# Optimization experiments

Hardware: AMD Instinct MI355X
Metric: run time of the kernel (lower is better)

Reference implementation:

```python
import jax, jax.numpy as jnp
import numpy as np

N = 512          # data_info['n']
K = 513          # data_info['k'] + 1
B = 65536        # batch size


def _build_adjust(n, k):
    # Reproduces the __init__ mask construction exactly.
    a1 = np.ones((n - 1, k - 1, 2), dtype=np.float32)
    a2 = np.zeros((n - 1, k - 1, 2), dtype=np.float32)
    for i in range(0, k - 2):
        if i >= n - 1:
            break
        f1 = a1[i].reshape(-1)
        f1[2 + 2 * i:] = 0
        a1[i] = f1.reshape(k - 1, 2)
        f2 = a2[i].reshape(-1)
        f2[2 + 2 * i + 1] = 1
        a2[i] = f2.reshape(k - 1, 2)
    return jnp.asarray(a1), jnp.asarray(a2)


W_ADJ1, W_ADJ2 = _build_adjust(N, K)


def setup_inputs() -> dict:
    key = jax.random.key(0)
    k1, k2, k3 = jax.random.split(key, 3)
    x = jax.random.randint(k1, (B, N), 0, 2, dtype=jnp.int32)
    W = jax.random.normal(k2, (N - 1, K - 1, 2), dtype=jnp.float32)
    endW = jax.random.normal(k3, (1, K), dtype=jnp.float32)
    return {"x": x, "W": W, "endW": endW}


def reference(x, W, endW):
    # W_full construction (softmax over the 2-way split, masked, with the
    # deterministic [1,0] row prepended along the group axis).
    Wsm = jax.nn.softmax(W, axis=2)                      # (n-1, k-1, 2)
    W_full = Wsm * W_ADJ1 + W_ADJ2                       # (n-1, k-1, 2)
    append = jnp.zeros((N - 1, 1, 2), W_full.dtype).at[:, :, 0].set(1.0)
    W_full = jnp.concatenate([append, W_full], axis=1)   # (n-1, k, 2)

    # group_num at step i is the running cumsum of x[:, 0..i]; the serial
    # recurrence collapses to a single cumsum, letting us gather all steps
    # at once instead of the original n-1 step Python loop.
    g = jnp.cumsum(x, axis=1)                            # (B, n)
    steps = jnp.arange(N - 1)                            # step i -> W_full[i-1]
    vals = W_full[steps[None, :], g[:, 1:], x[:, 1:]]    # (B, n-1)
    out = jnp.sum(jnp.log(vals), axis=1, keepdims=True)  # (B, 1)

    e = jax.nn.softmax(endW, axis=1)[0]                  # (k,)
    out = out + jnp.log(e[g[:, -1]])[:, None]            # (B, 1)
    return out
```

## Files before the change

kernel.cpp:

```cpp
#include <hip/hip_runtime.h>
#include <math.h>

#define NN      512
#define KK      513
#define BB      65536
#define TROWS   512
#define TCOLS   513
#define TSTRIDE (2 * TCOLS)

#define RPB     64
#define NSEG    8
#define SEGW    64
#define BLK     (RPB * NSEG)
#define XSTR    129

typedef int iv4 __attribute__((ext_vector_type(4)));

__global__ void build_table_kernel(const float* __restrict__ W, float* __restrict__ T) {
    int idx = blockIdx.x * blockDim.x + threadIdx.x;
    if (idx >= TROWS * TCOLS) return;
    int t = idx / TCOLS;
    int g = idx - t * TCOLS;
    float v0 = 0.f, v1 = 0.f;
    if (t >= 1 && g >= 1 && g <= t) {
        const float* w = W + ((size_t)(t - 1) * (KK - 1) + (g - 1)) * 2;
        float w0 = w[0], w1 = w[1];
        float m  = fmaxf(w0, w1);
        float lse = m + logf(expf(w0 - m) + expf(w1 - m));
        v0 = w0 - lse;
        v1 = w1 - lse;
    }
    T[2 * idx + 0] = v0;
    T[2 * idx + 1] = v1;
}

__global__ void build_endw_kernel(const float* __restrict__ endW, float* __restrict__ logE) {
    int lane = threadIdx.x;
    float vals[9];
    float m = -1e30f;
    #pragma unroll
    for (int k = 0; k < 9; ++k) {
        int i = lane + 64 * k;
        vals[k] = (i < KK) ? endW[i] : -1e30f;
        m = fmaxf(m, vals[k]);
    }
    #pragma unroll
    for (int d = 32; d >= 1; d >>= 1) m = fmaxf(m, __shfl_xor(m, d, 64));
    float s = 0.f;
    #pragma unroll
    for (int k = 0; k < 9; ++k) s += expf(vals[k] - m);
    #pragma unroll
    for (int d = 32; d >= 1; d >>= 1) s += __shfl_xor(s, d, 64);
    float lse = m + logf(s);
    #pragma unroll
    for (int k = 0; k < 9; ++k) {
        int i = lane + 64 * k;
        if (i < KK) logE[i] = endW[i] - lse;
    }
}

__global__ __launch_bounds__(BLK, 8) void pc_main_kernel(
    const int* __restrict__ x, const float* __restrict__ T,
    const float* __restrict__ logE, float* __restrict__ out)
{
    __shared__ unsigned int  xb[RPB * XSTR];
    __shared__ int           segsum[NSEG * RPB];
    __shared__ float         partial[NSEG * RPB];

    const int tid  = threadIdx.x;
    const int row0 = blockIdx.x * RPB;

    {
        const iv4* tile = (const iv4*)(x + (size_t)row0 * NN);
        #pragma unroll
        for (int j = 0; j < 16; ++j) {
            int i = tid + BLK * j;
            iv4 a = __builtin_nontemporal_load(&tile[i]);
            int r    = i >> 7;
            int col4 = i & 127;
            unsigned int m = (unsigned int)(a.x & 1)
                           | ((unsigned int)(a.y & 1) << 8)
                           | ((unsigned int)(a.z & 1) << 16)
                           | ((unsigned int)(a.w & 1) << 24);
            xb[r * XSTR + col4] = m;
        }
    }
    __syncthreads();

    const int seg  = tid >> 6;
    const int lane = tid & 63;

    unsigned int w[16];
    int ssum = 0;
    #pragma unroll
    for (int m = 0; m < 16; ++m) {
        w[m] = xb[lane * XSTR + seg * 16 + m];
        ssum += __popc(w[m]);
    }
    segsum[seg * 64 + lane] = ssum;
    __syncthreads();

    int g = 0, gtot = 0;
    #pragma unroll
    for (int s = 0; s < NSEG; ++s) {
        int v = segsum[s * 64 + lane];
        if (s < seg) g += v;
        gtot += v;
    }

    float a0 = 0.f, a1 = 0.f, a2 = 0.f, a3 = 0.f;
    const float* Tbase = T + (size_t)seg * SEGW * TSTRIDE;
    #pragma unroll
    for (int m = 0; m < 16; ++m) {
        const float* Tm = Tbase + (size_t)(4 * m) * TSTRIDE;
        unsigned int wm = w[m];
        {
            int b0 = wm & 1;         g += b0; a0 += Tm[0 * TSTRIDE + 2 * g + b0];
            int b1 = (wm >> 8)  & 1; g += b1; a1 += Tm[1 * TSTRIDE + 2 * g + b1];
            int b2 = (wm >> 16) & 1; g += b2; a2 += Tm[2 * TSTRIDE + 2 * g + b2];
            int b3 = (wm >> 24) & 1; g += b3; a3 += Tm[3 * TSTRIDE + 2 * g + b3];
        }
    }
    partial[seg * 64 + lane] = (a0 + a1) + (a2 + a3);
    __syncthreads();

    if (seg == 0) {
        float s = logE[gtot];
        #pragma unroll
        for (int t = 0; t < NSEG; ++t) s += partial[t * 64 + lane];
        out[row0 + lane] = s;
    }
}

extern "C" void kernel_launch(void* const* d_in, const int* in_sizes, int n_in,
                              void* d_out, int out_size, void* d_ws, size_t ws_size,
                              hipStream_t stream)
{
    const int*   x    = (const int*)d_in[0];
    const float* W    = (const float*)d_in[1];
    const float* endW = (const float*)d_in[2];
    float*       out  = (float*)d_out;

    float* T    = (float*)d_ws;
    float* logE = (float*)((char*)d_ws + (size_t)TROWS * TCOLS * 2 * sizeof(float));

    {
        int total  = TROWS * TCOLS;
        int blocks = (total + 255) / 256;
        build_table_kernel<<<blocks, 256, 0, stream>>>(W, T);
    }
    build_endw_kernel<<<1, 64, 0, stream>>>(endW, logE);
    pc_main_kernel<<<BB / RPB, BLK, 0, stream>>>(x, T, logE, out);
}
```

Baseline: 202.0 us.

## Pack log-prob table into bf16 pairs and double-buffer two row tiles per block

New measurement: 220.8 us. +9.3%, slower.

```diff
diff --git a/kernel.cpp b/kernel.cpp
--- a/kernel.cpp
+++ b/kernel.cpp
@@ -6,17 +6,23 @@
 #define BB      65536
 #define TROWS   512
 #define TCOLS   513
-#define TSTRIDE (2 * TCOLS)
+#define T16STR  528
 
 #define RPB     64
 #define NSEG    8
 #define SEGW    64
 #define BLK     (RPB * NSEG)
 #define XSTR    129
+#define TPB2    2
 
 typedef int iv4 __attribute__((ext_vector_type(4)));
 
-__global__ void build_table_kernel(const float* __restrict__ W, float* __restrict__ T) {
+__device__ __forceinline__ unsigned f2bf(float f) {
+    unsigned u = __float_as_uint(f);
+    return (u + 0x7fffu + ((u >> 16) & 1u)) >> 16;
+}
+
+__global__ void build_table_kernel(const float* __restrict__ W, unsigned* __restrict__ T16) {
     int idx = blockIdx.x * blockDim.x + threadIdx.x;
     if (idx >= TROWS * TCOLS) return;
     int t = idx / TCOLS;
@@ -30,8 +36,7 @@
         v0 = w0 - lse;
         v1 = w1 - lse;
     }
-    T[2 * idx + 0] = v0;
-    T[2 * idx + 1] = v1;
+    T16[t * T16STR + g] = f2bf(v0) | (f2bf(v1) << 16);
 }
 
 __global__ void build_endw_kernel(const float* __restrict__ endW, float* __restrict__ logE) {
@@ -59,76 +64,97 @@
     }
 }
 
-__global__ __launch_bounds__(BLK, 8) void pc_main_kernel(
-    const int* __restrict__ x, const float* __restrict__ T,
+__global__ __launch_bounds__(BLK, 4) void pc_main_kernel(
+    const int* __restrict__ x, const unsigned* __restrict__ T16,
     const float* __restrict__ logE, float* __restrict__ out)
 {
-    __shared__ unsigned int  xb[RPB * XSTR];
-    __shared__ int           segsum[NSEG * RPB];
-    __shared__ float         partial[NSEG * RPB];
+    __shared__ unsigned xb[2][RPB * XSTR];
+    __shared__ int      segsum[NSEG * RPB];
+    __shared__ float    partial[NSEG * RPB];
 
-    const int tid  = threadIdx.x;
-    const int row0 = blockIdx.x * RPB;
+    const int tid   = threadIdx.x;
+    const int seg   = tid >> 6;
+    const int lane  = tid & 63;
+    const int rowbb = blockIdx.x * (RPB * TPB2);
 
     {
-        const iv4* tile = (const iv4*)(x + (size_t)row0 * NN);
+        const iv4* tile = (const iv4*)(x + (size_t)rowbb * NN);
         #pragma unroll
         for (int j = 0; j < 16; ++j) {
             int i = tid + BLK * j;
             iv4 a = __builtin_nontemporal_load(&tile[i]);
-            int r    = i >> 7;
-            int col4 = i & 127;
-            unsigned int m = (unsigned int)(a.x & 1)
-                           | ((unsigned int)(a.y & 1) << 8)
-                           | ((unsigned int)(a.z & 1) << 16)
-                           | ((unsigned int)(a.w & 1) << 24);
-            xb[r * XSTR + col4] = m;
+            unsigned m = (unsigned)(a.x & 1) | ((unsigned)(a.y & 1) << 8)
+                       | ((unsigned)(a.z & 1) << 16) | ((unsigned)(a.w & 1) << 24);
+            xb[0][(i >> 7) * XSTR + (i & 127)] = m;
         }
     }
     __syncthreads();
 
-    const int seg  = tid >> 6;
-    const int lane = tid & 63;
+    int cur = 0;
+    iv4 S[16];
+    #pragma unroll
+    for (int t = 0; t < TPB2; ++t) {
+        const int row0 = rowbb + t * RPB;
 
-    unsigned int w[16];
-    int ssum = 0;
-    #pragma unroll
-    for (int m = 0; m < 16; ++m) {
-        w[m] = xb[lane * XSTR + seg * 16 + m];
-        ssum += __popc(w[m]);
-    }
-    segsum[seg * 64 + lane] = ssum;
-    __syncthreads();
+        if (t + 1 < TPB2) {
+            const iv4* tile = (const iv4*)(x + (size_t)(row0 + RPB) * NN);
+            #pragma unroll
+            for (int j = 0; j < 16; ++j) S[j] = __builtin_nontemporal_load(&tile[tid + BLK * j]);
+        }
 
-    int g = 0, gtot = 0;
-    #pragma unroll
-    for (int s = 0; s < NSEG; ++s) {
-        int v = segsum[s * 64 + lane];
-        if (s < seg) g += v;
-        gtot += v;
-    }
+        unsigned w[16];
+        int ssum = 0;
+        #pragma unroll
+        for (int m = 0; m < 16; ++m) {
+            w[m] = xb[cur][lane * XSTR + seg * 16 + m];
+            ssum += __popc(w[m]);
+        }
+        segsum[seg * 64 + lane] = ssum;
+        __syncthreads();
 
-    float a0 = 0.f, a1 = 0.f, a2 = 0.f, a3 = 0.f;
-    const float* Tbase = T + (size_t)seg * SEGW * TSTRIDE;
-    #pragma unroll
-    for (int m = 0; m < 16; ++m) {
-        const float* Tm = Tbase + (size_t)(4 * m) * TSTRIDE;
-        unsigned int wm = w[m];
-        {
-            int b0 = wm & 1;         g += b0; a0 += Tm[0 * TSTRIDE + 2 * g + b0];
-            int b1 = (wm >> 8)  & 1; g += b1; a1 += Tm[1 * TSTRIDE + 2 * g + b1];
-            int b2 = (wm >> 16) & 1; g += b2; a2 += Tm[2 * TSTRIDE + 2 * g + b2];
-            int b3 = (wm >> 24) & 1; g += b3; a3 += Tm[3 * TSTRIDE + 2 * g + b3];
+        int g = 0, gtot = 0;
+        #pragma unroll
+        for (int s = 0; s < NSEG; ++s) {
+            int v = segsum[s * 64 + lane];
+            if (s < seg) g += v;
+            gtot += v;
         }
-    }
-    partial[seg * 64 + lane] = (a0 + a1) + (a2 + a3);
-    __syncthreads();
 
-    if (seg == 0) {
-        float s = logE[gtot];
+        float a0 = 0.f, a1 = 0.f, a2 = 0.f, a3 = 0.f;
+        const unsigned* Tseg = T16 + (size_t)(seg * SEGW) * T16STR;
         #pragma unroll
-        for (int t = 0; t < NSEG; ++t) s += partial[t * 64 + lane];
-        out[row0 + lane] = s;
+        for (int m = 0; m < 16; ++m) {
+            const unsigned* Tm = Tseg + (size_t)(4 * m) * T16STR;
+            unsigned wm = w[m];
+            int b0 = wm & 1;         g += b0; unsigned u0 = Tm[0 * T16STR + g];
+            a0 += __uint_as_float(b0 ? (u0 & 0xffff0000u) : (u0 << 16));
+            int b1 = (wm >> 8)  & 1; g += b1; unsigned u1 = Tm[1 * T16STR + g];
+            a1 += __uint_as_float(b1 ? (u1 & 0xffff0000u) : (u1 << 16));
+            int b2 = (wm >> 16) & 1; g += b2; unsigned u2 = Tm[2 * T16STR + g];
+            a2 += __uint_as_float(b2 ? (u2 & 0xffff0000u) : (u2 << 16));
+            int b3 = (wm >> 24) & 1; g += b3; unsigned u3 = Tm[3 * T16STR + g];
+            a3 += __uint_as_float(b3 ? (u3 & 0xffff0000u) : (u3 << 16));
+        }
+        partial[seg * 64 + lane] = (a0 + a1) + (a2 + a3);
+
+        if (t + 1 < TPB2) {
+            #pragma unroll
+            for (int j = 0; j < 16; ++j) {
+                int i = tid + BLK * j;
+                unsigned m = (unsigned)(S[j].x & 1) | ((unsigned)(S[j].y & 1) << 8)
+                           | ((unsigned)(S[j].z & 1) << 16) | ((unsigned)(S[j].w & 1) << 24);
+                xb[cur ^ 1][(i >> 7) * XSTR + (i & 127)] = m;
+            }
+        }
+        __syncthreads();
+
+        if (seg == 0) {
+            float s = logE[gtot];
+            #pragma unroll
+            for (int q = 0; q < NSEG; ++q) s += partial[q * 64 + lane];
+            out[row0 + lane] = s;
+        }
+        cur ^= 1;
     }
 }
 
@@ -141,14 +167,14 @@
     const float* endW = (const float*)d_in[2];
     float*       out  = (float*)d_out;
 
-    float* T    = (float*)d_ws;
-    float* logE = (float*)((char*)d_ws + (size_t)TROWS * TCOLS * 2 * sizeof(float));
+    unsigned* T16  = (unsigned*)d_ws;
+    float*    logE = (float*)((char*)d_ws + (size_t)TROWS * T16STR * sizeof(unsigned));
 
     {
         int total  = TROWS * TCOLS;
         int blocks = (total + 255) / 256;
-        build_table_kernel<<<blocks, 256, 0, stream>>>(W, T);
+        build_table_kernel<<<blocks, 256, 0, stream>>>(W, T16);
     }
     build_endw_kernel<<<1, 64, 0, stream>>>(endW, logE);
-    pc_main_kernel<<<BB / RPB, BLK, 0, stream>>>(x, T, logE, out);
+    pc_main_kernel<<<BB / (RPB * TPB2), BLK, 0, stream>>>(x, T16, logE, out);
 }
```
